# Performance work log

Measured on AMD Instinct MI355X. Metric: run time of the kernel, lower is better.

## Reference

```python
import jax, jax.numpy as jnp
import numpy as np

N = 200000   # active voxels
B = 2        # batch size
G = 128      # spatial grid extent per axis
CIN = 64
COUT = 64
KS = 3       # kernel size -> 27 offsets
DIL = 1
EPS = 1e-5


def setup_inputs() -> dict:
    rng = np.random.default_rng(0)
    # unique active voxel coordinates over a B x G^3 grid
    lin = rng.choice(B * G * G * G, size=N, replace=False)
    b = lin // (G * G * G)
    r = lin % (G * G * G)
    x = r // (G * G)
    r2 = r % (G * G)
    y = r2 // G
    z = r2 % G
    coords = jnp.asarray(np.stack([b, x, y, z], axis=1).astype(np.int32))
    key = jax.random.key(0)
    ks = jax.random.split(key, 7)
    feats = jax.random.normal(ks[0], (N, CIN), jnp.float32)
    s1 = 1.0 / np.sqrt(KS ** 3 * CIN)
    s2 = 1.0 / np.sqrt(KS ** 3 * COUT)
    return {
        "feats": feats,
        "w1": jax.random.normal(ks[1], (KS ** 3, CIN, COUT), jnp.float32) * s1,
        "g1": 1.0 + 0.1 * jax.random.normal(ks[2], (COUT,), jnp.float32),
        "b1": 0.1 * jax.random.normal(ks[3], (COUT,), jnp.float32),
        "w2": jax.random.normal(ks[4], (KS ** 3, COUT, COUT), jnp.float32) * s2,
        "g2": 1.0 + 0.1 * jax.random.normal(ks[5], (COUT,), jnp.float32),
        "b2": 0.1 * jax.random.normal(ks[6], (COUT,), jnp.float32),
        "coords": coords,
    }


def build_neighbors(coords):
    """Hash (dense) lookup: for each of 27 kernel offsets, the input index of
    the neighboring active voxel (submanifold: output sites == input sites).
    Returns idx [27, N] int32 (0 where invalid) and mask [27, N] bool."""
    n = coords.shape[0]
    lin = ((coords[:, 0] * G + coords[:, 1]) * G + coords[:, 2]) * G + coords[:, 3]
    table = jnp.full((B * G * G * G,), -1, jnp.int32).at[lin].set(
        jnp.arange(n, dtype=jnp.int32))
    offs = jnp.asarray(
        [[dx, dy, dz] for dx in (-1, 0, 1) for dy in (-1, 0, 1) for dz in (-1, 0, 1)],
        dtype=jnp.int32) * DIL                       # [27, 3]
    nxyz = coords[None, :, 1:] + offs[:, None, :]    # [27, N, 3]
    inb = jnp.all((nxyz >= 0) & (nxyz < G), axis=-1)  # [27, N]
    c = jnp.clip(nxyz, 0, G - 1)
    nlin = ((coords[None, :, 0] * G + c[..., 0]) * G + c[..., 1]) * G + c[..., 2]
    idx = table[nlin]                                # [27, N]
    mask = inb & (idx >= 0)
    return jnp.where(mask, idx, 0), mask


def subm_conv(feats, nbr_idx, nbr_mask, w):
    # gather-GEMM-scatter, accumulated per kernel offset
    out = jnp.zeros((feats.shape[0], w.shape[-1]), feats.dtype)
    for k in range(w.shape[0]):
        g = jnp.where(nbr_mask[k][:, None], feats[nbr_idx[k]], 0.0)  # [N, Cin]
        out = out + g @ w[k]
    return out


def sparse_bn(x, gamma, beta):
    m = jnp.mean(x, axis=0)
    v = jnp.var(x, axis=0)
    return (x - m) * jax.lax.rsqrt(v + EPS) * gamma + beta


def reference(feats, w1, g1, b1, w2, g2, b2, coords):
    nbr_idx, nbr_mask = build_neighbors(coords)
    h = jax.nn.relu(sparse_bn(subm_conv(feats, nbr_idx, nbr_mask, w1), g1, b1))
    h = sparse_bn(subm_conv(h, nbr_idx, nbr_mask, w2), g2, b2)
    # shortcut is Identity (in_channels == out_channels, stride == 1)
    return jax.nn.relu(h + feats)
```

## Files before the change

### kernel.cpp

```cpp
#include <hip/hip_runtime.h>


constexpr int N_VOX = 200000;
constexpr int GEXT  = 128;
constexpr int C     = 64;
constexpr int K27   = 27;
constexpr int TBL_N = 2 * GEXT * GEXT * GEXT;
constexpr float EPSF = 1e-5f;

constexpr int NCH      = 782;
constexpr int PAIR_CAP = 460032;
constexpr int TIL64    = PAIR_CAP / 64;
constexpr int PBB      = 6250;
constexpr int RBLK     = 128;

using short8   = __attribute__((ext_vector_type(8))) short;
using floatx16 = __attribute__((ext_vector_type(16))) float;

static __device__ __forceinline__ ushort f2bf(float f) {
  union { float f; unsigned u; } a; a.f = f;
  unsigned r = a.u + 0x7fff + ((a.u >> 16) & 1);
  return (ushort)(r >> 16);
}
static __device__ __forceinline__ float bf2f(ushort h) {
  union { unsigned u; float f; } a; a.u = ((unsigned)h) << 16;
  return a.f;
}


__global__ __launch_bounds__(256) void k_fill(int* __restrict__ t,
                                              int* __restrict__ bsum,
                                              int* __restrict__ inl) {
  int i = blockIdx.x * 256 + threadIdx.x;
  if (i < TBL_N) t[i] = -1;
  if (i < 4096) bsum[i] = 0;
  if (i < PAIR_CAP) inl[i] = -1;
}

__global__ __launch_bounds__(256) void k_scatcnt(const int* __restrict__ coords,
                                                 int* __restrict__ t,
                                                 int* __restrict__ bsum) {
  int n = blockIdx.x * 256 + threadIdx.x;
  if (n >= N_VOX) return;
  int4 c = reinterpret_cast<const int4*>(coords)[n];
  int lin = ((c.x * GEXT + c.y) * GEXT + c.z) * GEXT + c.w;
  t[lin] = n;
  atomicAdd(&bsum[lin >> 10], 1);
}

__global__ __launch_bounds__(1024) void k_scan(const int* __restrict__ bsum,
                                               int* __restrict__ boff) {
  __shared__ int sc[1024];
  int t = threadIdx.x;
  int v0 = bsum[t * 4], v1 = bsum[t * 4 + 1], v2 = bsum[t * 4 + 2],
      v3 = bsum[t * 4 + 3];
  int s = v0 + v1 + v2 + v3;
  sc[t] = s;
  __syncthreads();
  for (int off = 1; off < 1024; off <<= 1) {
    int x = (t >= off) ? sc[t - off] : 0;
    __syncthreads();
    sc[t] += x;
    __syncthreads();
  }
  int excl = sc[t] - s;
  boff[t * 4]     = excl;
  boff[t * 4 + 1] = excl + v0;
  boff[t * 4 + 2] = excl + v0 + v1;
  boff[t * 4 + 3] = excl + v0 + v1 + v2;
}

__global__ __launch_bounds__(1024) void k_compact(int* __restrict__ table,
                                                  const int* __restrict__ boff,
                                                  int* __restrict__ perm) {
  __shared__ int wsum[16];
  int i = blockIdx.x * 1024 + threadIdx.x;
  int orig = table[i];
  bool valid = orig >= 0;
  unsigned long long bal = __ballot(valid);
  int lane = threadIdx.x & 63, wv = threadIdx.x >> 6;
  int before = __popcll(bal & ((1ull << lane) - 1ull));
  if (lane == 0) wsum[wv] = __popcll(bal);
  __syncthreads();
  int woff = 0;
  for (int w = 0; w < 16; ++w) woff += (w < wv) ? wsum[w] : 0;
  if (valid) {
    int j = boff[blockIdx.x] + woff + before;
    perm[j] = orig;
    table[i] = j;
  }
}

__global__ __launch_bounds__(256) void k_nbrc(const int* __restrict__ coords,
                                              const int* __restrict__ table,
                                              const int* __restrict__ perm,
                                              int* __restrict__ nbrp,
                                              int* __restrict__ cnt2) {
  __shared__ int wcnt[27][4];
  int tid = threadIdx.x;
  int j = blockIdx.x * 256 + tid;
  bool on = j < N_VOX;
  int4 c = {0, 0, 0, 0};
  if (on) {
    int orig = perm[j];
    c = reinterpret_cast<const int4*>(coords)[orig];
  }
  int k = 0;
  #pragma unroll
  for (int dx = -1; dx <= 1; ++dx)
    #pragma unroll
    for (int dy = -1; dy <= 1; ++dy)
      #pragma unroll
      for (int dz = -1; dz <= 1; ++dz) {
        int rank = -1;
        if (on) {
          int x = c.y + dx, y = c.z + dy, z = c.w + dz;
          if (((unsigned)x < (unsigned)GEXT) & ((unsigned)y < (unsigned)GEXT) &
              ((unsigned)z < (unsigned)GEXT)) {
            int lin = ((c.x * GEXT + x) * GEXT + y) * GEXT + z;
            rank = table[lin];
          }
          nbrp[k * N_VOX + j] = rank;
        }
        unsigned long long bal = __ballot(rank >= 0);
        if ((tid & 63) == 0) wcnt[k][tid >> 6] = __popcll(bal);
        ++k;
      }
  __syncthreads();
  if (tid < 27)
    cnt2[tid * NCH + blockIdx.x] =
        wcnt[tid][0] + wcnt[tid][1] + wcnt[tid][2] + wcnt[tid][3];
}

__global__ __launch_bounds__(256) void k_segscan(const int* __restrict__ cnt2,
                                                 int* __restrict__ choff,
                                                 int* __restrict__ segs) {
  __shared__ int sc[256];
  int k = blockIdx.x, t = threadIdx.x;
  int v[4];
  #pragma unroll
  for (int i = 0; i < 4; ++i) {
    int idx = t * 4 + i;
    v[i] = (idx < NCH) ? cnt2[k * NCH + idx] : 0;
  }
  int s = v[0] + v[1] + v[2] + v[3];
  sc[t] = s;
  __syncthreads();
  for (int off = 1; off < 256; off <<= 1) {
    int x = (t >= off) ? sc[t - off] : 0;
    __syncthreads();
    sc[t] += x;
    __syncthreads();
  }
  int run = sc[t] - s;
  #pragma unroll
  for (int i = 0; i < 4; ++i) {
    int idx = t * 4 + i;
    if (idx < NCH) choff[k * NCH + idx] = run;
    run += v[i];
  }
  if (t == 255) segs[k] = sc[255];
}

__global__ __launch_bounds__(1024) void k_tiles(int* __restrict__ segs,
                                                int* __restrict__ tile_k) {
  __shared__ int sb[28];
  if (threadIdx.x == 0) {
    int b = 0;
    for (int k = 0; k < K27; ++k) {
      sb[k] = b;
      segs[32 + k] = b;
      b += (segs[k] + 63) & ~63;
    }
    sb[27] = b;
    segs[32 + K27] = b;
  }
  __syncthreads();
  for (int t = threadIdx.x; t < TIL64; t += 1024) {
    int p0 = t * 64, kk = -1;
    #pragma unroll 1
    for (int k = 0; k < K27; ++k)
      if (p0 >= sb[k] && p0 < sb[k + 1]) kk = k;
    tile_k[t] = kk;
  }
}

__global__ __launch_bounds__(256) void k_pairs(int* __restrict__ nbrp,
                                               const int* __restrict__ choff,
                                               const int* __restrict__ segs,
                                               int* __restrict__ inl) {
  __shared__ int wsum[4];
  int k = blockIdx.x / NCH, cch = blockIdx.x % NCH;
  int j = cch * 256 + threadIdx.x;
  int v = (j < N_VOX) ? nbrp[k * N_VOX + j] : -1;
  bool valid = v >= 0;
  unsigned long long bal = __ballot(valid);
  int lane = threadIdx.x & 63, wv = threadIdx.x >> 6;
  int before = __popcll(bal & ((1ull << lane) - 1ull));
  if (lane == 0) wsum[wv] = __popcll(bal);
  __syncthreads();
  int woff = 0;
  #pragma unroll
  for (int w = 0; w < 4; ++w) woff += (w < wv) ? wsum[w] : 0;
  if (valid) {
    int p = segs[32 + k] + choff[k * NCH + cch] + woff + before;
    inl[p] = v;
    nbrp[k * N_VOX + j] = p;
  }
}


__global__ __launch_bounds__(256) void k_prep(const float* __restrict__ feats,
                                              const int* __restrict__ perm,
                                              const float* __restrict__ w1,
                                              const float* __restrict__ w2,
                                              ushort* __restrict__ fbp,
                                              ushort* __restrict__ wp1,
                                              ushort* __restrict__ wp2) {
  int b = blockIdx.x;
  if (b < 12500) {
    int i = b * 256 + threadIdx.x;
    int j = i >> 4, seg = i & 15;
    int p = perm[j];
    float4 v = reinterpret_cast<const float4*>(feats)[(p << 4) + seg];
    ushort4 o;
    o.x = f2bf(v.x); o.y = f2bf(v.y); o.z = f2bf(v.z); o.w = f2bf(v.w);
    reinterpret_cast<ushort4*>(fbp)[i] = o;
  } else {
    const float* w = (b < 12932) ? w1 : w2;
    ushort* wp = (b < 12932) ? wp1 : wp2;
    int i = (b - (b < 12932 ? 12500 : 12932)) * 256 + threadIdx.x;
    int k = i >> 12, r = i & 4095, ci = r >> 6, co = r & 63;
    int ch = co >> 5, row = co & 31;
    int ks = ci >> 4, hi1 = (ci >> 3) & 1, e = ci & 7;
    int dst = ((((k * 2 + ch) * 4 + ks) * 2 + hi1) << 8) + row * 8 + e;
    wp[dst] = f2bf(w[i]);
  }
}

template <bool APPLY_BN>
__global__ __launch_bounds__(256, 4) void k_pva(
    const ushort* __restrict__ fin,
    const ushort* __restrict__ wp,
    const int* __restrict__ inl,
    const int* __restrict__ tile_k,
    const float* __restrict__ ab,
    ushort* __restrict__ pv) {
  __shared__ float abl[128];
  const int kk = tile_k[blockIdx.x];
  const int tid = threadIdx.x;
  if (APPLY_BN) {
    if (tid < 128) abl[tid] = ab[tid];
    __syncthreads();
  }
  if (kk < 0) return;
  const int lane = tid & 63, wv = tid >> 6;
  const int lo = lane & 31, hi = lane >> 5;
  const int ch = wv & 1, vh = wv >> 1;
  const int pr = blockIdx.x * 64 + vh * 32 + lo;
  const int idx = inl[pr];

  const char* wk = (const char*)wp + (kk << 13) + (ch << 12) + (lane << 4);
  short8 a0 = *(const short8*)(wk);
  short8 a1 = *(const short8*)(wk + 1024);
  short8 a2 = *(const short8*)(wk + 2048);
  short8 a3 = *(const short8*)(wk + 3072);

  short8 b0, b1, b2, b3;
  if (idx >= 0) {
    const char* b = (const char*)fin + ((size_t)idx << 7) + (hi << 4);
    b0 = *(const short8*)(b);
    b1 = *(const short8*)(b + 32);
    b2 = *(const short8*)(b + 64);
    b3 = *(const short8*)(b + 96);
    if (APPLY_BN) {
      #pragma unroll
      for (int ks = 0; ks < 4; ++ks) {
        short8& v = ks == 0 ? b0 : ks == 1 ? b1 : ks == 2 ? b2 : b3;
        int cb = ks * 16 + hi * 8;
        #pragma unroll
        for (int e = 0; e < 8; ++e) {
          float x = bf2f((ushort)v[e]);
          x = fmaxf(x * abl[cb + e] + abl[64 + cb + e], 0.f);
          v[e] = (short)f2bf(x);
        }
      }
    }
  } else {
    b0 = short8{0,0,0,0,0,0,0,0}; b1 = b0; b2 = b0; b3 = b0;
  }

  floatx16 acc;
  #pragma unroll
  for (int j = 0; j < 16; ++j) acc[j] = 0.f;
  acc = __builtin_amdgcn_mfma_f32_32x32x16_bf16(a0, b0, acc, 0, 0, 0);
  acc = __builtin_amdgcn_mfma_f32_32x32x16_bf16(a1, b1, acc, 0, 0, 0);
  acc = __builtin_amdgcn_mfma_f32_32x32x16_bf16(a2, b2, acc, 0, 0, 0);
  acc = __builtin_amdgcn_mfma_f32_32x32x16_bf16(a3, b3, acc, 0, 0, 0);

  ushort* o = pv + ((size_t)pr << 6) + (ch << 5) + (hi << 2);
  #pragma unroll
  for (int rg = 0; rg < 4; ++rg) {
    ushort4 v;
    v.x = f2bf(acc[rg * 4 + 0]); v.y = f2bf(acc[rg * 4 + 1]);
    v.z = f2bf(acc[rg * 4 + 2]); v.w = f2bf(acc[rg * 4 + 3]);
    *(ushort4*)(o + (rg << 3)) = v;
  }
}

__global__ __launch_bounds__(256) void k_pvb(
    const ushort* __restrict__ pv,
    const int* __restrict__ pidx,
    ushort* __restrict__ fout,
    float* __restrict__ part) {
  __shared__ float sred[4][8][16];
  const int tid = threadIdx.x, lane = tid & 63, wv = tid >> 6;
  const int g = tid >> 3, e = tid & 7;
  const int j = blockIdx.x * 32 + g;

  int p[27];
  #pragma unroll
  for (int t = 0; t < K27; ++t) p[t] = pidx[t * N_VOX + j];

  float acc[8];
  #pragma unroll
  for (int r = 0; r < 8; ++r) acc[r] = 0.f;
  #pragma unroll
  for (int t = 0; t < K27; ++t) {
    if (p[t] >= 0) {
      short8 v = *(const short8*)(pv + ((size_t)p[t] << 6) + (e << 3));
      #pragma unroll
      for (int r = 0; r < 8; ++r) acc[r] += bf2f((ushort)v[r]);
    }
  }

  ushort* o = fout + ((size_t)j << 6) + (e << 3);
  ushort4 v0, v1;
  v0.x = f2bf(acc[0]); v0.y = f2bf(acc[1]);
  v0.z = f2bf(acc[2]); v0.w = f2bf(acc[3]);
  v1.x = f2bf(acc[4]); v1.y = f2bf(acc[5]);
  v1.z = f2bf(acc[6]); v1.w = f2bf(acc[7]);
  *(ushort4*)o = v0;
  *(ushort4*)(o + 4) = v1;

  #pragma unroll
  for (int r = 0; r < 8; ++r) {
    float s = acc[r], ss = acc[r] * acc[r];
    s += __shfl_xor(s, 8);  ss += __shfl_xor(ss, 8);
    s += __shfl_xor(s, 16); ss += __shfl_xor(ss, 16);
    s += __shfl_xor(s, 32); ss += __shfl_xor(ss, 32);
    if (lane < 8) { sred[wv][lane][r] = s; sred[wv][lane][8 + r] = ss; }
  }
  __syncthreads();
  if (tid < 128) {
    int half = tid >> 6, chn = tid & 63;
    int e2 = chn >> 3, r2 = chn & 7;
    float v = sred[0][e2][half * 8 + r2] + sred[1][e2][half * 8 + r2] +
              sred[2][e2][half * 8 + r2] + sred[3][e2][half * 8 + r2];
    part[(size_t)blockIdx.x * 128 + tid] = v;
  }
}


__global__ __launch_bounds__(256) void k_red(const float* __restrict__ part,
                                             float* __restrict__ part2) {
  __shared__ float red[256];
  int tid = threadIdx.x;
  int e = tid & 127, g = tid >> 7;
  float s = 0.f;
  for (int r = blockIdx.x * 2 + g; r < PBB; r += 2 * RBLK)
    s += part[(size_t)r * 128 + e];
  red[tid] = s;
  __syncthreads();
  if (tid < 128) part2[(size_t)blockIdx.x * 128 + tid] = red[tid] + red[tid + 128];
}

__global__ __launch_bounds__(256) void k_bnfin(const float* __restrict__ part2,
                                               const float* __restrict__ gamma,
                                               const float* __restrict__ beta,
                                               float* __restrict__ ab) {
  __shared__ float fin[128];
  int tid = threadIdx.x;
  if (tid < 128) {
    float s = 0.f;
    for (int r = 0; r < RBLK; ++r) s += part2[(size_t)r * 128 + tid];
    fin[tid] = s;
  }
  __syncthreads();
  if (tid < 64) {
    float su = fin[tid], ss = fin[64 + tid];
    float mean = su / (float)N_VOX;
    float var  = ss / (float)N_VOX - mean * mean;
    float a = gamma[tid] * rsqrtf(var + EPSF);
    ab[tid]      = a;
    ab[64 + tid] = beta[tid] - mean * a;
  }
}

__global__ __launch_bounds__(256) void k_final(const ushort* __restrict__ h2p,
                                               const float* __restrict__ feats,
                                               const int* __restrict__ perm,
                                               const float* __restrict__ ab,
                                               float* __restrict__ out) {
  int i = blockIdx.x * 256 + threadIdx.x;
  int j = i >> 4, seg = i & 15;
  int p = perm[j];
  ushort4 h = reinterpret_cast<const ushort4*>(h2p)[i];
  float4 f = reinterpret_cast<const float4*>(feats)[(p << 4) + seg];
  int cb = seg * 4;
  float4 o;
  o.x = fmaxf(bf2f(h.x) * ab[cb]     + ab[64 + cb]     + f.x, 0.f);
  o.y = fmaxf(bf2f(h.y) * ab[cb + 1] + ab[64 + cb + 1] + f.y, 0.f);
  o.z = fmaxf(bf2f(h.z) * ab[cb + 2] + ab[64 + cb + 2] + f.z, 0.f);
  o.w = fmaxf(bf2f(h.w) * ab[cb + 3] + ab[64 + cb + 3] + f.w, 0.f);
  reinterpret_cast<float4*>(out)[(p << 4) + seg] = o;
}

extern "C" void kernel_launch(void* const* d_in, const int* in_sizes, int n_in,
                              void* d_out, int out_size, void* d_ws, size_t ws_size,
                              hipStream_t stream) {
  const float* feats  = (const float*)d_in[0];
  const float* w1     = (const float*)d_in[1];
  const float* g1     = (const float*)d_in[2];
  const float* b1     = (const float*)d_in[3];
  const float* w2     = (const float*)d_in[4];
  const float* g2     = (const float*)d_in[5];
  const float* b2     = (const float*)d_in[6];
  const int*   coords = (const int*)d_in[7];
  float* out = (float*)d_out;

  char* ws = (char*)d_ws;
  ushort* pv    = (ushort*)ws;  ws += (size_t)PAIR_CAP * C * 2;
  int*    table = (int*)ws;     ws += (size_t)TBL_N * 4;
  int*    nbrp  = (int*)ws;     ws += (size_t)K27 * N_VOX * 4;
  ushort* fbp   = (ushort*)ws;  ws += (size_t)N_VOX * C * 2;
  ushort* h1p   = (ushort*)ws;  ws += (size_t)N_VOX * C * 2;
  int*    perm  = (int*)ws;     ws += (size_t)N_VOX * 4;
  ushort* wp1   = (ushort*)ws;  ws += (size_t)K27 * 4096 * 2;
  ushort* wp2   = (ushort*)ws;  ws += (size_t)K27 * 4096 * 2;
  int*    inl   = (int*)ws;     ws += (size_t)PAIR_CAP * 4;
  int*    bsum  = (int*)ws;     ws += 4096 * 4;
  int*    boff  = (int*)ws;     ws += 4096 * 4;
  int*    cnt2  = (int*)ws;     ws += (size_t)K27 * NCH * 4;
  int*    choff = (int*)ws;     ws += (size_t)K27 * NCH * 4;
  int*    segs  = (int*)ws;     ws += 256;
  int*    tilk  = (int*)ws;     ws += (size_t)TIL64 * 4;
  float*  part2 = (float*)ws;   ws += (size_t)RBLK * 128 * 4;
  float*  ab1   = (float*)ws;   ws += 512;
  float*  ab2   = (float*)ws;   ws += 512;
  float*  part  = (float*)table;
  ushort* h2p   = fbp;

  k_fill<<<TBL_N / 256, 256, 0, stream>>>(table, bsum, inl);
  k_scatcnt<<<(N_VOX + 255) / 256, 256, 0, stream>>>(coords, table, bsum);
  k_scan<<<1, 1024, 0, stream>>>(bsum, boff);
  k_compact<<<TBL_N / 1024, 1024, 0, stream>>>(table, boff, perm);
  k_nbrc<<<NCH, 256, 0, stream>>>(coords, table, perm, nbrp, cnt2);
  k_segscan<<<K27, 256, 0, stream>>>(cnt2, choff, segs);
  k_tiles<<<1, 1024, 0, stream>>>(segs, tilk);
  k_pairs<<<K27 * NCH, 256, 0, stream>>>(nbrp, choff, segs, inl);

  k_prep<<<13364, 256, 0, stream>>>(feats, perm, w1, w2, fbp, wp1, wp2);

  k_pva<false><<<TIL64, 256, 0, stream>>>(fbp, wp1, inl, tilk, ab1, pv);
  k_pvb<<<PBB, 256, 0, stream>>>(pv, nbrp, h1p, part);
  k_red<<<RBLK, 256, 0, stream>>>(part, part2);
  k_bnfin<<<1, 256, 0, stream>>>(part2, g1, b1, ab1);

  k_pva<true><<<TIL64, 256, 0, stream>>>(h1p, wp2, inl, tilk, ab1, pv);
  k_pvb<<<PBB, 256, 0, stream>>>(pv, nbrp, h2p, part);
  k_red<<<RBLK, 256, 0, stream>>>(part, part2);
  k_bnfin<<<1, 256, 0, stream>>>(part2, g2, b2, ab2);

  k_final<<<N_VOX * 16 / 256, 256, 0, stream>>>(h2p, feats, perm, ab2, out);
}
```

Before: 298.6 us.

## Fuse pair compaction with prep, drop tile map, stage pva stores via LDS

Merges the pair-compaction kernel and the bf16 feature/weight prep kernel into one launch. The tile-to-offset kernel is removed, and each block now recomputes its segment base from segs, so the -1 fill of inl is dropped and a per-row count check is used instead. k_pva now writes its output tile through swizzled shared memory so the global stores are coalesced 128-byte rows. k_final reads the residual from the bf16 permuted copy rather than gathering fp32 feats, which needs a separate h2p buffer and trades residual precision for less traffic.

```diff
diff --git a/kernel.cpp b/kernel.cpp
--- a/kernel.cpp
+++ b/kernel.cpp
@@ -13,6 +13,9 @@
 constexpr int TIL64    = PAIR_CAP / 64;
 constexpr int PBB      = 6250;
 constexpr int RBLK     = 128;
+constexpr int PAIRS_BLKS = K27 * NCH;
+constexpr int PREP_FEAT  = 12500;
+constexpr int PREP_W     = 432;
 
 using short8   = __attribute__((ext_vector_type(8))) short;
 using floatx16 = __attribute__((ext_vector_type(16))) float;
@@ -29,12 +32,10 @@
 
 
 __global__ __launch_bounds__(256) void k_fill(int* __restrict__ t,
-                                              int* __restrict__ bsum,
-                                              int* __restrict__ inl) {
+                                              int* __restrict__ bsum) {
   int i = blockIdx.x * 256 + threadIdx.x;
   if (i < TBL_N) t[i] = -1;
   if (i < 4096) bsum[i] = 0;
-  if (i < PAIR_CAP) inl[i] = -1;
 }
 
 __global__ __launch_bounds__(256) void k_scatcnt(const int* __restrict__ coords,
@@ -162,64 +163,41 @@
   if (t == 255) segs[k] = sc[255];
 }
 
-__global__ __launch_bounds__(1024) void k_tiles(int* __restrict__ segs,
-                                                int* __restrict__ tile_k) {
-  __shared__ int sb[28];
-  if (threadIdx.x == 0) {
-    int b = 0;
-    for (int k = 0; k < K27; ++k) {
-      sb[k] = b;
-      segs[32 + k] = b;
-      b += (segs[k] + 63) & ~63;
+__global__ __launch_bounds__(256) void k_pairs_prep(
+    int* __restrict__ nbrp, const int* __restrict__ choff,
+    const int* __restrict__ segs, int* __restrict__ inl,
+    const float* __restrict__ feats, const int* __restrict__ perm,
+    const float* __restrict__ w1, const float* __restrict__ w2,
+    ushort* __restrict__ fbp, ushort* __restrict__ wp1,
+    ushort* __restrict__ wp2) {
+  int b = blockIdx.x;
+  if (b < PAIRS_BLKS) {
+    __shared__ int wsum[4];
+    int k = b / NCH, cch = b % NCH;
+    int base = 0;
+    #pragma unroll 1
+    for (int kk = 0; kk < K27; ++kk) {
+      if (kk == k) break;
+      base += (segs[kk] + 63) & ~63;
     }
-    sb[27] = b;
-    segs[32 + K27] = b;
-  }
-  __syncthreads();
-  for (int t = threadIdx.x; t < TIL64; t += 1024) {
-    int p0 = t * 64, kk = -1;
-    #pragma unroll 1
-    for (int k = 0; k < K27; ++k)
-      if (p0 >= sb[k] && p0 < sb[k + 1]) kk = k;
-    tile_k[t] = kk;
-  }
-}
-
-__global__ __launch_bounds__(256) void k_pairs(int* __restrict__ nbrp,
-                                               const int* __restrict__ choff,
-                                               const int* __restrict__ segs,
-                                               int* __restrict__ inl) {
-  __shared__ int wsum[4];
-  int k = blockIdx.x / NCH, cch = blockIdx.x % NCH;
-  int j = cch * 256 + threadIdx.x;
-  int v = (j < N_VOX) ? nbrp[k * N_VOX + j] : -1;
-  bool valid = v >= 0;
-  unsigned long long bal = __ballot(valid);
-  int lane = threadIdx.x & 63, wv = threadIdx.x >> 6;
-  int before = __popcll(bal & ((1ull << lane) - 1ull));
-  if (lane == 0) wsum[wv] = __popcll(bal);
-  __syncthreads();
-  int woff = 0;
-  #pragma unroll
-  for (int w = 0; w < 4; ++w) woff += (w < wv) ? wsum[w] : 0;
-  if (valid) {
-    int p = segs[32 + k] + choff[k * NCH + cch] + woff + before;
-    inl[p] = v;
-    nbrp[k * N_VOX + j] = p;
-  }
-}
-
-
-__global__ __launch_bounds__(256) void k_prep(const float* __restrict__ feats,
-                                              const int* __restrict__ perm,
-                                              const float* __restrict__ w1,
-                                              const float* __restrict__ w2,
-                                              ushort* __restrict__ fbp,
-                                              ushort* __restrict__ wp1,
-                                              ushort* __restrict__ wp2) {
-  int b = blockIdx.x;
-  if (b < 12500) {
-    int i = b * 256 + threadIdx.x;
+    int j = cch * 256 + threadIdx.x;
+    int v = (j < N_VOX) ? nbrp[k * N_VOX + j] : -1;
+    bool valid = v >= 0;
+    unsigned long long bal = __ballot(valid);
+    int lane = threadIdx.x & 63, wv = threadIdx.x >> 6;
+    int before = __popcll(bal & ((1ull << lane) - 1ull));
+    if (lane == 0) wsum[wv] = __popcll(bal);
+    __syncthreads();
+    int woff = 0;
+    #pragma unroll
+    for (int w = 0; w < 4; ++w) woff += (w < wv) ? wsum[w] : 0;
+    if (valid) {
+      int p = base + choff[k * NCH + cch] + woff + before;
+      inl[p] = v;
+      nbrp[k * N_VOX + j] = p;
+    }
+  } else if (b < PAIRS_BLKS + PREP_FEAT) {
+    int i = (b - PAIRS_BLKS) * 256 + threadIdx.x;
     int j = i >> 4, seg = i & 15;
     int p = perm[j];
     float4 v = reinterpret_cast<const float4*>(feats)[(p << 4) + seg];
@@ -227,9 +205,10 @@
     o.x = f2bf(v.x); o.y = f2bf(v.y); o.z = f2bf(v.z); o.w = f2bf(v.w);
     reinterpret_cast<ushort4*>(fbp)[i] = o;
   } else {
-    const float* w = (b < 12932) ? w1 : w2;
-    ushort* wp = (b < 12932) ? wp1 : wp2;
-    int i = (b - (b < 12932 ? 12500 : 12932)) * 256 + threadIdx.x;
+    int b2 = b - PAIRS_BLKS - PREP_FEAT;
+    const float* w = (b2 < PREP_W) ? w1 : w2;
+    ushort* wp = (b2 < PREP_W) ? wp1 : wp2;
+    int i = (b2 < PREP_W ? b2 : b2 - PREP_W) * 256 + threadIdx.x;
     int k = i >> 12, r = i & 4095, ci = r >> 6, co = r & 63;
     int ch = co >> 5, row = co & 31;
     int ks = ci >> 4, hi1 = (ci >> 3) & 1, e = ci & 7;
@@ -243,22 +222,35 @@
     const ushort* __restrict__ fin,
     const ushort* __restrict__ wp,
     const int* __restrict__ inl,
-    const int* __restrict__ tile_k,
+    const int* __restrict__ segs,
     const float* __restrict__ ab,
     ushort* __restrict__ pv) {
+  __shared__ ushort tile[64 * 64];
   __shared__ float abl[128];
-  const int kk = tile_k[blockIdx.x];
   const int tid = threadIdx.x;
+  const int p0 = blockIdx.x * 64;
+
+  int base = 0, kk = -1, off = 0, cnt = 0;
+  #pragma unroll 1
+  for (int k = 0; k < K27; ++k) {
+    int raw = segs[k];
+    int padded = (raw + 63) & ~63;
+    if (p0 >= base && p0 < base + padded) { kk = k; off = base; cnt = raw; }
+    base += padded;
+  }
+  if (kk < 0) return;
+
   if (APPLY_BN) {
     if (tid < 128) abl[tid] = ab[tid];
     __syncthreads();
   }
-  if (kk < 0) return;
+
   const int lane = tid & 63, wv = tid >> 6;
   const int lo = lane & 31, hi = lane >> 5;
   const int ch = wv & 1, vh = wv >> 1;
-  const int pr = blockIdx.x * 64 + vh * 32 + lo;
-  const int idx = inl[pr];
+  const int pr = p0 + vh * 32 + lo;
+  const bool vld = (pr - off) < cnt;
+  const int idx = vld ? inl[pr] : -1;
 
   const char* wk = (const char*)wp + (kk << 13) + (ch << 12) + (lane << 4);
   short8 a0 = *(const short8*)(wk);
@@ -298,13 +290,26 @@
   acc = __builtin_amdgcn_mfma_f32_32x32x16_bf16(a2, b2, acc, 0, 0, 0);
   acc = __builtin_amdgcn_mfma_f32_32x32x16_bf16(a3, b3, acc, 0, 0, 0);
 
-  ushort* o = pv + ((size_t)pr << 6) + (ch << 5) + (hi << 2);
-  #pragma unroll
-  for (int rg = 0; rg < 4; ++rg) {
-    ushort4 v;
-    v.x = f2bf(acc[rg * 4 + 0]); v.y = f2bf(acc[rg * 4 + 1]);
-    v.z = f2bf(acc[rg * 4 + 2]); v.w = f2bf(acc[rg * 4 + 3]);
-    *(ushort4*)(o + (rg << 3)) = v;
+  {
+    int r = vh * 32 + lo, rx = r & 7;
+    char* trow = (char*)tile + r * 128 + hi * 8;
+    #pragma unroll
+    for (int rg = 0; rg < 4; ++rg) {
+      ushort4 v;
+      v.x = f2bf(acc[rg * 4 + 0]); v.y = f2bf(acc[rg * 4 + 1]);
+      v.z = f2bf(acc[rg * 4 + 2]); v.w = f2bf(acc[rg * 4 + 3]);
+      *(ushort4*)(trow + (((ch * 4 + rg) ^ rx) << 4)) = v;
+    }
+  }
+  __syncthreads();
+  {
+    int row = tid >> 2, rx = row & 7, chunk = tid & 3;
+    const char* src = (const char*)tile + row * 128;
+    uint4 x = *(const uint4*)(src + (((chunk * 2) ^ rx) << 4));
+    uint4 y = *(const uint4*)(src + (((chunk * 2 + 1) ^ rx) << 4));
+    char* dst = (char*)pv + ((size_t)(p0 + row) << 7) + chunk * 32;
+    *(uint4*)(dst) = x;
+    *(uint4*)(dst + 16) = y;
   }
 }
 
@@ -398,7 +403,7 @@
 }
 
 __global__ __launch_bounds__(256) void k_final(const ushort* __restrict__ h2p,
-                                               const float* __restrict__ feats,
+                                               const ushort* __restrict__ fbp,
                                                const int* __restrict__ perm,
                                                const float* __restrict__ ab,
                                                float* __restrict__ out) {
@@ -406,13 +411,13 @@
   int j = i >> 4, seg = i & 15;
   int p = perm[j];
   ushort4 h = reinterpret_cast<const ushort4*>(h2p)[i];
-  float4 f = reinterpret_cast<const float4*>(feats)[(p << 4) + seg];
+  ushort4 f = reinterpret_cast<const ushort4*>(fbp)[i];
   int cb = seg * 4;
   float4 o;
-  o.x = fmaxf(bf2f(h.x) * ab[cb]     + ab[64 + cb]     + f.x, 0.f);
-  o.y = fmaxf(bf2f(h.y) * ab[cb + 1] + ab[64 + cb + 1] + f.y, 0.f);
-  o.z = fmaxf(bf2f(h.z) * ab[cb + 2] + ab[64 + cb + 2] + f.z, 0.f);
-  o.w = fmaxf(bf2f(h.w) * ab[cb + 3] + ab[64 + cb + 3] + f.w, 0.f);
+  o.x = fmaxf(bf2f(h.x) * ab[cb]     + ab[64 + cb]     + bf2f(f.x), 0.f);
+  o.y = fmaxf(bf2f(h.y) * ab[cb + 1] + ab[64 + cb + 1] + bf2f(f.y), 0.f);
+  o.z = fmaxf(bf2f(h.z) * ab[cb + 2] + ab[64 + cb + 2] + bf2f(f.z), 0.f);
+  o.w = fmaxf(bf2f(h.w) * ab[cb + 3] + ab[64 + cb + 3] + bf2f(f.w), 0.f);
   reinterpret_cast<float4*>(out)[(p << 4) + seg] = o;
 }
 
@@ -435,6 +440,7 @@
   int*    nbrp  = (int*)ws;     ws += (size_t)K27 * N_VOX * 4;
   ushort* fbp   = (ushort*)ws;  ws += (size_t)N_VOX * C * 2;
   ushort* h1p   = (ushort*)ws;  ws += (size_t)N_VOX * C * 2;
+  ushort* h2p   = (ushort*)ws;  ws += (size_t)N_VOX * C * 2;
   int*    perm  = (int*)ws;     ws += (size_t)N_VOX * 4;
   ushort* wp1   = (ushort*)ws;  ws += (size_t)K27 * 4096 * 2;
   ushort* wp2   = (ushort*)ws;  ws += (size_t)K27 * 4096 * 2;
@@ -444,33 +450,29 @@
   int*    cnt2  = (int*)ws;     ws += (size_t)K27 * NCH * 4;
   int*    choff = (int*)ws;     ws += (size_t)K27 * NCH * 4;
   int*    segs  = (int*)ws;     ws += 256;
-  int*    tilk  = (int*)ws;     ws += (size_t)TIL64 * 4;
   float*  part2 = (float*)ws;   ws += (size_t)RBLK * 128 * 4;
   float*  ab1   = (float*)ws;   ws += 512;
   float*  ab2   = (float*)ws;   ws += 512;
   float*  part  = (float*)table;
-  ushort* h2p   = fbp;
-
-  k_fill<<<TBL_N / 256, 256, 0, stream>>>(table, bsum, inl);
+
+  k_fill<<<TBL_N / 256, 256, 0, stream>>>(table, bsum);
   k_scatcnt<<<(N_VOX + 255) / 256, 256, 0, stream>>>(coords, table, bsum);
   k_scan<<<1, 1024, 0, stream>>>(bsum, boff);
   k_compact<<<TBL_N / 1024, 1024, 0, stream>>>(table, boff, perm);
   k_nbrc<<<NCH, 256, 0, stream>>>(coords, table, perm, nbrp, cnt2);
   k_segscan<<<K27, 256, 0, stream>>>(cnt2, choff, segs);
-  k_tiles<<<1, 1024, 0, stream>>>(segs, tilk);
-  k_pairs<<<K27 * NCH, 256, 0, stream>>>(nbrp, choff, segs, inl);
-
-  k_prep<<<13364, 256, 0, stream>>>(feats, perm, w1, w2, fbp, wp1, wp2);
-
-  k_pva<false><<<TIL64, 256, 0, stream>>>(fbp, wp1, inl, tilk, ab1, pv);
+  k_pairs_prep<<<PAIRS_BLKS + PREP_FEAT + 2 * PREP_W, 256, 0, stream>>>(
+      nbrp, choff, segs, inl, feats, perm, w1, w2, fbp, wp1, wp2);
+
+  k_pva<false><<<TIL64, 256, 0, stream>>>(fbp, wp1, inl, segs, ab1, pv);
   k_pvb<<<PBB, 256, 0, stream>>>(pv, nbrp, h1p, part);
   k_red<<<RBLK, 256, 0, stream>>>(part, part2);
   k_bnfin<<<1, 256, 0, stream>>>(part2, g1, b1, ab1);
 
-  k_pva<true><<<TIL64, 256, 0, stream>>>(h1p, wp2, inl, tilk, ab1, pv);
+  k_pva<true><<<TIL64, 256, 0, stream>>>(h1p, wp2, inl, segs, ab1, pv);
   k_pvb<<<PBB, 256, 0, stream>>>(pv, nbrp, h2p, part);
   k_red<<<RBLK, 256, 0, stream>>>(part, part2);
   k_bnfin<<<1, 256, 0, stream>>>(part2, g2, b2, ab2);
 
-  k_final<<<N_VOX * 16 / 256, 256, 0, stream>>>(h2p, feats, perm, ab2, out);
-}
+  k_final<<<N_VOX * 16 / 256, 256, 0, stream>>>(h2p, fbp, perm, ab2, out);
+}
```

Measured after the change: 277.3 us. 1.08x faster.
